# Kernel optimization log

Hardware: AMD Instinct MI355X
Metric: run time of the kernel (lower is better)

The kernel has to match this reference:

```python
import jax, jax.numpy as jnp
import numpy as np

ROIALIGN = (7, 7)   # args.roialign_size
SCALE = 0.125       # args.spatial_scale
SR = 2              # roi_align sampling ratio (fixed; torchvision uses adaptive when -1)


def _conv2d(x, w, b, pad):
    y = jax.lax.conv_general_dilated(x, w, (1, 1), pad,
                                     dimension_numbers=('NCHW', 'OIHW', 'NCHW'))
    return y + b[None, :, None, None]


def _bilinear(f, ys, xs):
    # f: [C,H,W]; ys: [Ny]; xs: [Nx] -> [C,Ny,Nx]
    C, H, W = f.shape
    y = jnp.clip(ys, 0.0, H - 1.0)
    x = jnp.clip(xs, 0.0, W - 1.0)
    y0 = jnp.floor(y).astype(jnp.int32)
    x0 = jnp.floor(x).astype(jnp.int32)
    y1 = jnp.minimum(y0 + 1, H - 1)
    x1 = jnp.minimum(x0 + 1, W - 1)
    wy = (y - y0)[None, :, None]
    wx = (x - x0)[None, None, :]
    f00 = f[:, y0[:, None], x0[None, :]]
    f01 = f[:, y0[:, None], x1[None, :]]
    f10 = f[:, y1[:, None], x0[None, :]]
    f11 = f[:, y1[:, None], x1[None, :]]
    return f00 * (1 - wy) * (1 - wx) + f01 * (1 - wy) * wx + f10 * wy * (1 - wx) + f11 * wy * wx


def _roi_align(feat, rois):
    # feat: [N,C,H,W]; rois: [K,5] = (batch_idx, x1, y1, x2, y2) in image coords
    rh, rw = ROIALIGN
    C = feat.shape[1]

    def one(box, bidx):
        f = feat[bidx]
        x1, y1, x2, y2 = box * SCALE
        bh = (y2 - y1) / rh
        bw = (x2 - x1) / rw
        ys = y1 + (jnp.arange(rh * SR, dtype=feat.dtype) + 0.5) / SR * bh
        xs = x1 + (jnp.arange(rw * SR, dtype=feat.dtype) + 0.5) / SR * bw
        s = _bilinear(f, ys, xs)                       # [C, rh*SR, rw*SR]
        return s.reshape(C, rh, SR, rw, SR).mean(axis=(2, 4))

    return jax.vmap(one)(rois[:, 1:5], rois[:, 0].astype(jnp.int32))


def setup_inputs() -> dict:
    key = jax.random.key(0)
    ks = jax.random.split(key, 16)
    N, M, H, W = 4, 48, 96, 96
    cor_planes = 4 * (2 * 4 + 1) ** 2  # 324
    corr = jax.random.normal(ks[0], (N, cor_planes, H, W), jnp.float32)

    def make_det(k):
        k1, k2, k3, k4, k5, k6 = jax.random.split(k, 6)
        cx = jax.random.uniform(k1, (N, M), minval=80.0, maxval=688.0)
        cy = jax.random.uniform(k2, (N, M), minval=80.0, maxval=688.0)
        w = jax.random.uniform(k3, (N, M), minval=24.0, maxval=120.0)
        h = jax.random.uniform(k4, (N, M), minval=24.0, maxval=120.0)
        valid = jnp.where(jax.random.uniform(k5, (N, M)) < 0.9, 1.0, -1.0)
        ids = jax.random.randint(k6, (N, M), 0, 100).astype(jnp.float32)
        pad = jnp.zeros((N, M, 4), jnp.float32)
        cols = [valid, ids, cx, cy, w, h]
        return jnp.concatenate([c[..., None] for c in cols] + [pad], axis=-1)

    detection1 = make_det(ks[1])
    detection2 = make_det(ks[2])

    def p(k, shape):
        return (jax.random.normal(k, shape, jnp.float32) * 0.02)

    return {
        'corr': corr,
        'detection1_': detection1,
        'detection1': detection1,
        'detection2': detection2,
        'convc1_w': p(ks[3], (256, cor_planes, 1, 1)), 'convc1_b': jnp.zeros(256, jnp.float32),
        'convc2_w': p(ks[4], (256, 256, 3, 3)), 'convc2_b': jnp.zeros(256, jnp.float32),
        'conv_w': p(ks[5], (128, 256, 3, 3)), 'conv_b': jnp.zeros(128, jnp.float32),
        'head_conv_w': p(ks[6], (256, 132, 7, 7)), 'head_conv_b': jnp.zeros(256, jnp.float32),
        'fc6_w': p(ks[7], (256, 256)), 'fc6_b': jnp.zeros(256, jnp.float32),
        'fc7_w': p(ks[8], (256, 256)), 'fc7_b': jnp.zeros(256, jnp.float32),
        'cls_w': p(ks[9], (1, 256)), 'cls_b': jnp.zeros(1, jnp.float32),
    }


def reference(corr, detection1_, detection1, detection2,
              convc1_w, convc1_b, convc2_w, convc2_b, conv_w, conv_b,
              head_conv_w, head_conv_b, fc6_w, fc6_b, fc7_w, fc7_b, cls_w, cls_b):
    N, M = detection1.shape[0], detection1.shape[1]
    rh, rw = ROIALIGN
    # CompressConv
    c = jax.nn.relu(_conv2d(corr, convc1_w, convc1_b, 'VALID'))
    c = jax.nn.relu(_conv2d(c, convc2_w, convc2_b, [(1, 1), (1, 1)]))
    rel = jax.nn.relu(_conv2d(c, conv_w, conv_b, [(1, 1), (1, 1)]))   # [N,128,H,W]

    def to_xyxy(d):
        xy1 = d[..., 2:4] - d[..., 4:6] / 2
        xy2 = xy1 + d[..., 4:6]
        return jnp.concatenate([d[..., :2], xy1, xy2, d[..., 6:]], axis=-1)

    d1 = to_xyxy(detection1)
    d2 = to_xyxy(detection2)
    bidx = jnp.broadcast_to(jnp.arange(N, dtype=d1.dtype)[:, None], (N, M))
    rois = jnp.concatenate([bidx[..., None], d1[..., 2:6]], axis=-1).reshape(N * M, 5)
    rf = _roi_align(rel, rois)                                        # [N*M,128,7,7]

    d_ = jnp.concatenate([
        jnp.broadcast_to(d1[..., :8][:, :, None, :], (N, M, M, 8)),
        jnp.broadcast_to(d2[..., :8][:, None, :, :], (N, M, M, 8)),
    ], axis=-1).reshape(N * M * M, 16)

    # position encoding: 4 relative-geometry channels tiled over the ROI grid
    eps = 1e-6
    cx1 = (d_[:, 2] + d_[:, 4]) * 0.5; cy1 = (d_[:, 3] + d_[:, 5]) * 0.5
    w1 = jnp.maximum(d_[:, 4] - d_[:, 2], eps); h1 = jnp.maximum(d_[:, 5] - d_[:, 3], eps)
    cx2 = (d_[:, 10] + d_[:, 12]) * 0.5; cy2 = (d_[:, 11] + d_[:, 13]) * 0.5
    w2 = jnp.maximum(d_[:, 12] - d_[:, 10], eps); h2 = jnp.maximum(d_[:, 13] - d_[:, 11], eps)
    pos4 = jnp.stack([(cx2 - cx1) / w1, (cy2 - cy1) / h1,
                      jnp.log(w2 / w1), jnp.log(h2 / h1)], axis=-1)   # [NMM,4]
    pos = jnp.broadcast_to(pos4[:, :, None, None], (N * M * M, 4, rh, rw))

    rf_exp = jnp.broadcast_to(rf[:, None], (N * M, M, 128, rh, rw)).reshape(N * M * M, 128, rh, rw)
    data = jnp.concatenate([rf_exp, pos], axis=1)                     # [NMM,132,7,7]

    labels = (d_[:, 1] == d_[:, 9]).astype(jnp.float32)
    valid = (d_[:, 0] != -1) & (d_[:, 8] != -1)

    # ConvMLPHead (scores for invalid pairs are simply masked out by `valid`)
    x = _conv2d(data, head_conv_w, head_conv_b, 'VALID').reshape(N * M * M, -1)
    x = jax.nn.relu(x @ fc6_w.T + fc6_b)
    x = jax.nn.relu(x @ fc7_w.T + fc7_b)
    scores = x @ cls_w.T + cls_b                                      # [NMM,1]
    return scores, labels, valid
```

## Files before the change

kernel.cpp:

```cpp
#include <hip/hip_runtime.h>
#include <hip/hip_bf16.h>

#define NB    4
#define HH    96
#define WW    96
#define PIX   9216
#define C0    324
#define MM    48
#define NROI  192
#define NPAIR 9216
#define KHEAD 6468
#define KRF   6272
#define SPLITS 28
#define CPS    7

#define CWSTG 18432

typedef unsigned short u16;
typedef __attribute__((ext_vector_type(8))) short bf16x8;
typedef __attribute__((ext_vector_type(4))) float f32x4;
typedef __attribute__((ext_vector_type(16))) float f32x16;
typedef __attribute__((ext_vector_type(4))) unsigned short u16x4;
typedef __attribute__((ext_vector_type(8))) unsigned short u16x8;
typedef __attribute__((ext_vector_type(4))) int i32x4;

__device__ __forceinline__ u16 f2bf(float f) {
    __hip_bfloat16 h = __float2bfloat16(f);
    union { __hip_bfloat16 h; u16 u; } c; c.h = h; return c.u;
}
__device__ __forceinline__ float b2f(u16 u) {
    union { unsigned int i; float f; } c; c.i = ((unsigned int)u) << 16; return c.f;
}

__global__ __launch_bounds__(256) void prep_v2(
    const float* __restrict__ c1w, const float* __restrict__ c2w,
    const float* __restrict__ c3w, const float* __restrict__ hw,
    const float* __restrict__ f6w, const float* __restrict__ f7w,
    u16* __restrict__ wt1f, u16* __restrict__ wt2f, u16* __restrict__ wt3f,
    u16* __restrict__ wtHt, u16* __restrict__ w6c, u16* __restrict__ w7c,
    float* __restrict__ wsum4, u16* __restrict__ a1, u16* __restrict__ a2)
{
    __shared__ u16 L[18432];
    const int blk = blockIdx.x, tid = threadIdx.x;

    if (blk < 8) {
        const int ot = blk;
        const float* src = c1w + (size_t)ot * 32 * C0;
        for (int it = 0; it < 11; ++it) {
            int i = tid + it * 256;
            if (i < 2592) {
                float4 v = *(const float4*)(src + i * 4);
                int n = i / 81, k4 = (i % 81) * 4;
                L[n * 324 + k4 + 0] = f2bf(v.x);
                L[n * 324 + k4 + 1] = f2bf(v.y);
                L[n * 324 + k4 + 2] = f2bf(v.z);
                L[n * 324 + k4 + 3] = f2bf(v.w);
            }
        }
        __syncthreads();
        for (int it = 0; it < 6; ++it) {
            int v = tid + it * 256;
            if (v >= 1408) break;
            int ks = v >> 6, lane = v & 63;
            int n = lane & 31, half = lane >> 5;
            u16x8 pk;
            #pragma unroll
            for (int j = 0; j < 8; ++j) {
                int k = ks * 16 + half * 8 + j;
                pk[j] = (k < C0) ? L[n * 324 + k] : (u16)0;
            }
            *(u16x8*)&wt1f[((ks * 8 + ot) * 64 + lane) * 8] = pk;
        }
    } else if (blk < 56) {
        const bool is2 = blk < 40;
        const int b8 = is2 ? (blk - 8) : (blk - 40);
        const int oc8 = b8 * 8;
        const int ocb = oc8 >> 7;
        const int ot = (oc8 >> 5) & 3;
        const int nb = oc8 & 31;
        const float* src = (is2 ? c2w : c3w) + (size_t)oc8 * 2304;
        u16* dst = is2 ? wt2f : wt3f;
        for (int it = 0; it < 18; ++it) {
            int i = tid + it * 256;
            float4 v = *(const float4*)(src + i * 4);
            int n = i / 576, t4 = (i % 576) * 4;
            L[n * 2304 + t4 + 0] = f2bf(v.x);
            L[n * 2304 + t4 + 1] = f2bf(v.y);
            L[n * 2304 + t4 + 2] = f2bf(v.z);
            L[n * 2304 + t4 + 3] = f2bf(v.w);
        }
        __syncthreads();
        for (int it = 0; it < 9; ++it) {
            int v = tid + it * 256;
            int o8 = v & 7; int rest = v >> 3;
            int half = rest & 1; rest >>= 1;
            int tap = rest % 9; int icb = rest / 9;
            int lane = half * 32 + nb + o8;
            u16x8 pk;
            #pragma unroll
            for (int j = 0; j < 8; ++j) {
                int ic = icb * 16 + half * 8 + j;
                pk[j] = L[o8 * 2304 + ic * 9 + tap];
            }
            size_t dest = ((((size_t)(ocb * 16 + icb) * 9 + tap) * 4 + ot) * 64 + lane) * 8;
            *(u16x8*)&dst[dest] = pk;
        }
    } else if (blk < 312) {
        const int oc = blk - 56;
        const float* src = hw + (size_t)oc * KHEAD;
        for (int it = 0; it < 7; ++it) {
            int i = tid + it * 256;
            if (i < 1617) {
                float4 v = *(const float4*)(src + i * 4);
                L[i * 4 + 0] = f2bf(v.x);
                L[i * 4 + 1] = f2bf(v.y);
                L[i * 4 + 2] = f2bf(v.z);
                L[i * 4 + 3] = f2bf(v.w);
            }
        }
        if (tid < 4) {
            const float* p = src + (128 + tid) * 49;
            float s = 0.f;
            #pragma unroll
            for (int t = 0; t < 49; ++t) s += p[t];
            wsum4[oc * 4 + tid] = s;
        }
        __syncthreads();
        for (int it = 0; it < 4; ++it) {
            int v = tid + it * 256;
            if (v >= 784) break;
            u16x8 pk;
            #pragma unroll
            for (int j = 0; j < 8; ++j) {
                int r = v * 8 + j;
                int s = r >> 7, c = r & 127;
                pk[j] = L[c * 49 + s];
            }
            *(u16x8*)&wtHt[(size_t)oc * KRF + v * 8] = pk;
        }
    } else if (blk < 344) {
        const bool is6 = blk < 328;
        const int b = is6 ? (blk - 312) : (blk - 328);
        const float* src = (is6 ? f6w : f7w) + (size_t)(b * 256 + tid) * 16;
        u16* dst = (is6 ? w6c : w7c) + (size_t)(b * 256 + tid) * 16;
        u16x8 pk0, pk1;
        #pragma unroll
        for (int h = 0; h < 2; ++h) {
            float4 v0 = *(const float4*)(src + h * 8);
            float4 v1 = *(const float4*)(src + h * 8 + 4);
            u16x8 pk;
            pk[0] = f2bf(v0.x); pk[1] = f2bf(v0.y); pk[2] = f2bf(v0.z); pk[3] = f2bf(v0.w);
            pk[4] = f2bf(v1.x); pk[5] = f2bf(v1.y); pk[6] = f2bf(v1.z); pk[7] = f2bf(v1.w);
            if (h == 0) pk0 = pk; else pk1 = pk;
        }
        *(u16x8*)(dst + 0) = pk0;
        *(u16x8*)(dst + 8) = pk1;
    } else {
        int idx = (blk - 344) * 256 + tid;
        int c8 = idx & 31;
        int t = idx >> 5;
        int h = t % 388, img = t / 388;
        u16* base = (img & 4) ? a2 : a1;
        int b = img & 3;
        int y, x;
        if (h < 98)       { y = 0;  x = h; }
        else if (h < 196) { y = 97; x = h - 98; }
        else { int r = (h - 196) >> 1; x = ((h - 196) & 1) * 97; y = 1 + r; }
        long long off = (((long long)(b * 98 + y)) * 98 + x) * 256 + c8 * 8;
        i32x4 z = {0, 0, 0, 0};
        *(i32x4*)(base + off) = z;
    }
}

__global__ __launch_bounds__(256) void conv1_v2(
    const float* __restrict__ corr, const u16* __restrict__ wf,
    const float* __restrict__ bias, u16* __restrict__ outp)
{
    __shared__ __align__(16) u16 Ws1[8192];
    __shared__ __align__(16) u16 Bs[64 * 40];
    const int tid = threadIdx.x;
    const int b = blockIdx.y;
    const int p0 = blockIdx.x * 64;
    const int lane = tid & 63, wid = tid >> 6;
    const int n = lane & 31, half = lane >> 5;
    const int wocw = wid & 1, wpx = wid >> 1;
    const int kr = tid >> 3, pxg = tid & 7;

    f32x16 acc[4];
    #pragma unroll
    for (int i = 0; i < 4; ++i)
        #pragma unroll
        for (int e = 0; e < 16; ++e) acc[i][e] = 0.f;

    float4 s0 = {0,0,0,0}, s1 = {0,0,0,0};
    if (kr < C0) {
        const float* src = &corr[((long long)(b * C0 + kr)) * PIX + p0 + pxg * 8];
        s0 = *(const float4*)src; s1 = *(const float4*)(src + 4);
    }
    bf16x8 wr[4];
    #pragma unroll
    for (int i = 0; i < 4; ++i) wr[i] = *(const bf16x8*)(wf + (i * 256 + tid) * 8);

    for (int kc = 0; kc < 11; ++kc) {
        __syncthreads();
        Bs[(pxg * 8 + 0) * 40 + kr] = f2bf(s0.x);
        Bs[(pxg * 8 + 1) * 40 + kr] = f2bf(s0.y);
        Bs[(pxg * 8 + 2) * 40 + kr] = f2bf(s0.z);
        Bs[(pxg * 8 + 3) * 40 + kr] = f2bf(s0.w);
        Bs[(pxg * 8 + 4) * 40 + kr] = f2bf(s1.x);
        Bs[(pxg * 8 + 5) * 40 + kr] = f2bf(s1.y);
        Bs[(pxg * 8 + 6) * 40 + kr] = f2bf(s1.z);
        Bs[(pxg * 8 + 7) * 40 + kr] = f2bf(s1.w);
        #pragma unroll
        for (int i = 0; i < 4; ++i) *(bf16x8*)&Ws1[(i * 256 + tid) * 8] = wr[i];
        __syncthreads();
        if (kc < 10) {
            int k = (kc + 1) * 32 + kr;
            if (k < C0) {
                const float* src = &corr[((long long)(b * C0 + k)) * PIX + p0 + pxg * 8];
                s0 = *(const float4*)src; s1 = *(const float4*)(src + 4);
            } else { s0 = (float4){0,0,0,0}; s1 = (float4){0,0,0,0}; }
            const u16* wn = wf + (kc + 1) * 8192;
            #pragma unroll
            for (int i = 0; i < 4; ++i) wr[i] = *(const bf16x8*)(wn + (i * 256 + tid) * 8);
        }
        #pragma unroll
        for (int ks = 0; ks < 2; ++ks) {
            bf16x8 bb = *(const bf16x8*)&Bs[(wpx * 32 + n) * 40 + ks * 16 + half * 8];
            #pragma unroll
            for (int ot = 0; ot < 4; ++ot) {
                bf16x8 a = *(const bf16x8*)&Ws1[((ks * 8 + wocw * 4 + ot) * 64 + lane) * 8];
                acc[ot] = __builtin_amdgcn_mfma_f32_32x32x16_bf16(a, bb, acc[ot], 0, 0, 0);
            }
        }
    }
    const int px = p0 + wpx * 32 + n;
    const int y = px / 96, x = px % 96;
    const long long obase = (((long long)(b * 98 + y + 1)) * 98 + x + 1) * 256;
    #pragma unroll
    for (int ot = 0; ot < 4; ++ot) {
        int ocb = wocw * 128 + ot * 32;
        f32x16 d = acc[ot];
        #pragma unroll
        for (int r2 = 0; r2 < 4; ++r2) {
            int oc4 = ocb + r2 * 8 + half * 4;
            f32x4 bv = *(const f32x4*)(bias + oc4);
            u16x4 pk;
            #pragma unroll
            for (int g = 0; g < 4; ++g) pk[g] = f2bf(fmaxf(d[r2 * 4 + g] + bv[g], 0.f));
            *(u16x4*)(outp + obase + oc4) = pk;
        }
    }
}

template<int COUT, bool PADOUT>
__global__ __launch_bounds__(256, 2) void conv3x3_v3(
    const u16* __restrict__ inp, const u16* __restrict__ wf,
    const float* __restrict__ bias, u16* __restrict__ outp)
{
    __shared__ __align__(16) u16 Ws[CWSTG];
    __shared__ __align__(16) u16 Hs[204 * 24];
    const int tid = threadIdx.x;
    const int b = blockIdx.z;
    const int x0 = (blockIdx.x % 3) * 32, y0 = (blockIdx.x / 3) * 4;
    const int lane = tid & 63, wid = tid >> 6;
    const int n = lane & 31, half = lane >> 5;
    const int woc = wid & 1, wpx = wid >> 1;

    const u16* wsrc = wf + (size_t)blockIdx.y * 16 * CWSTG;
    const bool hstager = tid < 204;
    const int hrow = tid / 34, hcol = tid % 34;
    const u16* hsrc = inp + (((size_t)(b * 98 + y0 + hrow)) * 98 + x0 + hcol) * 256;

    f32x16 acc[2][2];
    #pragma unroll
    for (int i = 0; i < 2; ++i)
        #pragma unroll
        for (int r = 0; r < 2; ++r)
            #pragma unroll
            for (int e = 0; e < 16; ++e) acc[i][r][e] = 0.f;

    bf16x8 wreg[9];
    bf16x8 h0, h1;
    #pragma unroll
    for (int it = 0; it < 9; ++it)
        wreg[it] = *(const bf16x8*)(wsrc + (it * 256 + tid) * 8);
    if (hstager) { h0 = *(const bf16x8*)hsrc; h1 = *(const bf16x8*)(hsrc + 8); }

    for (int icb = 0; icb < 16; ++icb) {
        __syncthreads();
        #pragma unroll
        for (int it = 0; it < 9; ++it)
            *(bf16x8*)&Ws[(it * 256 + tid) * 8] = wreg[it];
        if (hstager) {
            *(bf16x8*)&Hs[tid * 24]     = h0;
            *(bf16x8*)&Hs[tid * 24 + 8] = h1;
        }
        __syncthreads();
        if (icb < 15) {
            const u16* wn = wsrc + (size_t)(icb + 1) * CWSTG;
            #pragma unroll
            for (int it = 0; it < 9; ++it)
                wreg[it] = *(const bf16x8*)(wn + (it * 256 + tid) * 8);
            if (hstager) {
                const u16* hn = hsrc + (icb + 1) * 16;
                h0 = *(const bf16x8*)hn; h1 = *(const bf16x8*)(hn + 8);
            }
        }
        bf16x8 afr[9][2];
        #pragma unroll
        for (int tap = 0; tap < 9; ++tap)
            #pragma unroll
            for (int j = 0; j < 2; ++j)
                afr[tap][j] = *(const bf16x8*)&Ws[((tap * 4 + woc * 2 + j) * 64 + lane) * 8];
        bf16x8 bfr[4][3];
        #pragma unroll
        for (int rr = 0; rr < 4; ++rr)
            #pragma unroll
            for (int dx = 0; dx < 3; ++dx)
                bfr[rr][dx] = *(const bf16x8*)&Hs[((wpx * 2 + rr) * 34 + dx + n) * 24 + half * 8];
        #pragma unroll
        for (int tap = 0; tap < 9; ++tap) {
            const int dy = tap / 3, dx = tap % 3;
            #pragma unroll
            for (int r = 0; r < 2; ++r) {
                acc[0][r] = __builtin_amdgcn_mfma_f32_32x32x16_bf16(afr[tap][0], bfr[r + dy][dx], acc[0][r], 0, 0, 0);
                acc[1][r] = __builtin_amdgcn_mfma_f32_32x32x16_bf16(afr[tap][1], bfr[r + dy][dx], acc[1][r], 0, 0, 0);
            }
        }
    }
    #pragma unroll
    for (int ot = 0; ot < 2; ++ot) {
        int ocb = blockIdx.y * 128 + woc * 64 + ot * 32;
        #pragma unroll
        for (int r = 0; r < 2; ++r) {
            int y = y0 + wpx * 2 + r;
            int x = x0 + n;
            f32x16 d = acc[ot][r];
            long long obase;
            if (PADOUT) obase = (((long long)(b * 98 + y + 1)) * 98 + x + 1) * COUT;
            else        obase = (((long long)(b * 96 + y)) * 96 + x) * COUT;
            #pragma unroll
            for (int r2 = 0; r2 < 4; ++r2) {
                int oc4 = ocb + r2 * 8 + half * 4;
                f32x4 bv = *(const f32x4*)(bias + oc4);
                u16x4 pk;
                #pragma unroll
                for (int g = 0; g < 4; ++g) pk[g] = f2bf(fmaxf(d[r2 * 4 + g] + bv[g], 0.f));
                *(u16x4*)(outp + obase + oc4) = pk;
            }
        }
    }
}

__global__ __launch_bounds__(256) void roi_align_cl(
    const u16* __restrict__ rel, const float* __restrict__ det1,
    u16* __restrict__ rf)
{
    const int roi = blockIdx.x, tid = threadIdx.x;
    const int c = tid & 127, sb = tid >> 7;
    const int b = roi / MM, m = roi % MM;
    const float* d = det1 + (long long)(b * MM + m) * 10;
    float cx = d[2], cy = d[3], w = d[4], h = d[5];
    float x1f = cx - w * 0.5f, y1f = cy - h * 0.5f;
    float x1 = x1f * 0.125f, y1 = y1f * 0.125f;
    float x2 = (x1f + w) * 0.125f, y2 = (y1f + h) * 0.125f;
    float bh = (y2 - y1) * (1.f / 7.f), bw = (x2 - x1) * (1.f / 7.f);
    const u16* fb = rel + (long long)b * PIX * 128 + c;
    for (int s = sb; s < 49; s += 2) {
        int i = s / 7, j = s % 7;
        float sum = 0.f;
        #pragma unroll
        for (int di = 0; di < 2; ++di) {
            float y = y1 + ((float)(2 * i + di) + 0.5f) * 0.5f * bh;
            y = fminf(fmaxf(y, 0.f), 95.f);
            int yy0 = (int)floorf(y);
            int yy1 = min(yy0 + 1, 95);
            float wy = y - (float)yy0;
            #pragma unroll
            for (int dj = 0; dj < 2; ++dj) {
                float x = x1 + ((float)(2 * j + dj) + 0.5f) * 0.5f * bw;
                x = fminf(fmaxf(x, 0.f), 95.f);
                int xx0 = (int)floorf(x);
                int xx1 = min(xx0 + 1, 95);
                float wx = x - (float)xx0;
                float f00 = b2f(fb[((long long)yy0 * 96 + xx0) * 128]);
                float f01 = b2f(fb[((long long)yy0 * 96 + xx1) * 128]);
                float f10 = b2f(fb[((long long)yy1 * 96 + xx0) * 128]);
                float f11 = b2f(fb[((long long)yy1 * 96 + xx1) * 128]);
                sum += f00 * (1.f - wy) * (1.f - wx) + f01 * (1.f - wy) * wx
                     + f10 * wy * (1.f - wx) + f11 * wy * wx;
            }
        }
        rf[(long long)roi * KRF + s * 128 + c] = f2bf(sum * 0.25f);
    }
}

__global__ __launch_bounds__(256) void head_gemm_mfma(
    const u16* __restrict__ rf, const u16* __restrict__ wtHt,
    float* __restrict__ Gpart)
{
    __shared__ __align__(16) u16 As[64 * 40];
    __shared__ __align__(16) u16 Bs[128 * 40];
    const int tid = threadIdx.x;
    const int rb = blockIdx.x >> 1, ob = blockIdx.x & 1;
    const int split = blockIdx.y;
    const int lane = tid & 63, wid = tid >> 6;
    const int q = lane >> 4, m16 = lane & 15;
    const int wr = wid & 1, wo = wid >> 1;

    const int arl = tid >> 2, aqd = tid & 3;
    const u16* abase = rf + (long long)(rb * 64 + arl) * KRF + aqd * 8;
    const int bol0 = tid >> 2, bqd = tid & 3;
    const u16* bbase0 = wtHt + (long long)(ob * 128 + bol0) * KRF + bqd * 8;
    const u16* bbase1 = bbase0 + 64LL * KRF;

    f32x4 acc[2][4];
    #pragma unroll
    for (int i = 0; i < 2; ++i)
        #pragma unroll
        for (int j = 0; j < 4; ++j) acc[i][j] = (f32x4){0.f, 0.f, 0.f, 0.f};

    int k0 = split * CPS * 32;
    bf16x8 ra = *(const bf16x8*)(abase + k0);
    bf16x8 rb0 = *(const bf16x8*)(bbase0 + k0);
    bf16x8 rb1 = *(const bf16x8*)(bbase1 + k0);
    for (int cch = 0; cch < CPS; ++cch) {
        __syncthreads();
        *(bf16x8*)&As[arl * 40 + aqd * 8] = ra;
        *(bf16x8*)&Bs[bol0 * 40 + bqd * 8] = rb0;
        *(bf16x8*)&Bs[(64 + bol0) * 40 + bqd * 8] = rb1;
        __syncthreads();
        if (cch < CPS - 1) {
            int kn = k0 + (cch + 1) * 32;
            ra  = *(const bf16x8*)(abase + kn);
            rb0 = *(const bf16x8*)(bbase0 + kn);
            rb1 = *(const bf16x8*)(bbase1 + kn);
        }
        bf16x8 a[2], bb[4];
        #pragma unroll
        for (int rt = 0; rt < 2; ++rt)
            a[rt] = *(const bf16x8*)&As[(wr * 32 + rt * 16 + m16) * 40 + q * 8];
        #pragma unroll
        for (int ot = 0; ot < 4; ++ot)
            bb[ot] = *(const bf16x8*)&Bs[(wo * 64 + ot * 16 + m16) * 40 + q * 8];
        #pragma unroll
        for (int rt = 0; rt < 2; ++rt)
            #pragma unroll
            for (int ot = 0; ot < 4; ++ot)
                acc[rt][ot] = __builtin_amdgcn_mfma_f32_16x16x32_bf16(a[rt], bb[ot], acc[rt][ot], 0, 0, 0);
    }
    #pragma unroll
    for (int rt = 0; rt < 2; ++rt)
        #pragma unroll
        for (int ot = 0; ot < 4; ++ot) {
            int oc = ob * 128 + wo * 64 + ot * 16 + m16;
            #pragma unroll
            for (int rg = 0; rg < 4; ++rg) {
                int roi = rb * 64 + wr * 32 + rt * 16 + q * 4 + rg;
                Gpart[((long long)split * NROI + roi) * 256 + oc] = acc[rt][ot][rg];
            }
        }
}

#define PHS 272
__global__ __launch_bounds__(256) void pair_head(
    const float* __restrict__ Gpart, const float* __restrict__ d1,
    const float* __restrict__ d2, const float* __restrict__ wsum4,
    const float* __restrict__ hb,
    const u16* __restrict__ w6, const float* __restrict__ b6,
    const u16* __restrict__ w7, const float* __restrict__ b7,
    const float* __restrict__ cw, const float* __restrict__ cb,
    float* __restrict__ scores, float* __restrict__ labels,
    float* __restrict__ valid)
{
    __shared__ __align__(16) u16 bufA[64 * PHS];
    __shared__ __align__(16) u16 bufB[64 * PHS];
    __shared__ float Gs[2][256];
    __shared__ float ps[64][4];
    __shared__ float clw[256];

    const int tid = threadIdx.x;
    const int p0 = blockIdx.x * 64;
    const int r0 = p0 / MM;
    const int lane = tid & 63, w = tid >> 6;
    const int q = lane >> 4, m16 = lane & 15;

    clw[tid] = cw[tid];
    #pragma unroll
    for (int l = 0; l < 2; ++l) {
        int idx = tid + l * 256;
        int rr = idx >> 8, col = idx & 255;
        int roi = min(r0 + rr, NROI - 1);
        float s = 0.f;
        #pragma unroll
        for (int sp = 0; sp < SPLITS; ++sp)
            s += Gpart[((long long)sp * NROI + roi) * 256 + col];
        Gs[rr][col] = s;
    }
    if (tid < 64) {
        int pair = p0 + tid;
        int b = pair / (MM * MM); int rem = pair % (MM * MM);
        int m1 = rem / MM, m2 = rem % MM;
        const float* rA = d1 + (long long)(b * MM + m1) * 10;
        const float* rB = d2 + (long long)(b * MM + m2) * 10;
        float v1 = rA[0], id1 = rA[1], cxa = rA[2], cya = rA[3], wa = rA[4], ha = rA[5];
        float v2 = rB[0], id2 = rB[1], cxb = rB[2], cyb = rB[3], wb = rB[4], hbv = rB[5];
        const float eps = 1e-6f;
        float ax1 = cxa - wa * 0.5f, ay1 = cya - ha * 0.5f;
        float ax2 = ax1 + wa,        ay2 = ay1 + ha;
        float bx1 = cxb - wb * 0.5f, by1 = cyb - hbv * 0.5f;
        float bx2 = bx1 + wb,        by2 = by1 + hbv;
        float ccx1 = (ax1 + ax2) * 0.5f, ccy1 = (ay1 + ay2) * 0.5f;
        float ww1 = fmaxf(ax2 - ax1, eps), hh1 = fmaxf(ay2 - ay1, eps);
        float ccx2 = (bx1 + bx2) * 0.5f, ccy2 = (by1 + by2) * 0.5f;
        float ww2 = fmaxf(bx2 - bx1, eps), hh2 = fmaxf(by2 - by1, eps);
        ps[tid][0] = (ccx2 - ccx1) / ww1;
        ps[tid][1] = (ccy2 - ccy1) / hh1;
        ps[tid][2] = logf(ww2 / ww1);
        ps[tid][3] = logf(hh2 / hh1);
        labels[pair] = (id1 == id2) ? 1.f : 0.f;
        valid[pair]  = (v1 != -1.f && v2 != -1.f) ? 1.f : 0.f;
    }
    __syncthreads();

    #pragma unroll
    for (int it = 0; it < 16; ++it) {
        int idx = tid + it * 256;
        int px = idx >> 6, o4 = (idx & 63) * 4;
        int rl = (p0 + px) / MM - r0;
        f32x4 g = *(const f32x4*)&Gs[rl][o4];
        f32x4 hv = *(const f32x4*)&hb[o4];
        f32x4 p4 = *(const f32x4*)&ps[px][0];
        u16x4 pk;
        #pragma unroll
        for (int j = 0; j < 4; ++j) {
            f32x4 w4 = *(const f32x4*)&wsum4[(o4 + j) * 4];
            float v = g[j] + hv[j] + p4[0] * w4[0] + p4[1] * w4[1] + p4[2] * w4[2] + p4[3] * w4[3];
            pk[j] = f2bf(v);
        }
        *(u16x4*)&bufA[px * PHS + o4] = pk;
    }
    __syncthreads();

    #pragma unroll
    for (int layer = 0; layer < 2; ++layer) {
        const u16* wgt = layer ? w7 : w6;
        const float* bs = layer ? b7 : b6;
        const u16* src = layer ? bufB : bufA;
        u16* dst = layer ? bufA : bufB;
        f32x4 acc[4][4];
        #pragma unroll
        for (int i = 0; i < 4; ++i)
            #pragma unroll
            for (int j = 0; j < 4; ++j) acc[i][j] = (f32x4){0.f, 0.f, 0.f, 0.f};
        #pragma unroll
        for (int kc = 0; kc < 8; ++kc) {
            bf16x8 a[4], bb[4];
            #pragma unroll
            for (int i = 0; i < 4; ++i)
                a[i] = *(const bf16x8*)&wgt[(w * 64 + i * 16 + m16) * 256 + kc * 32 + q * 8];
            #pragma unroll
            for (int pt = 0; pt < 4; ++pt)
                bb[pt] = *(const bf16x8*)&src[(pt * 16 + m16) * PHS + kc * 32 + q * 8];
            #pragma unroll
            for (int i = 0; i < 4; ++i)
                #pragma unroll
                for (int pt = 0; pt < 4; ++pt)
                    acc[i][pt] = __builtin_amdgcn_mfma_f32_16x16x32_bf16(a[i], bb[pt], acc[i][pt], 0, 0, 0);
        }
        #pragma unroll
        for (int i = 0; i < 4; ++i) {
            int oc4 = w * 64 + i * 16 + q * 4;
            f32x4 bv = *(const f32x4*)(bs + oc4);
            #pragma unroll
            for (int pt = 0; pt < 4; ++pt) {
                int px = pt * 16 + m16;
                f32x4 dd = acc[i][pt];
                u16x4 pk;
                #pragma unroll
                for (int rg = 0; rg < 4; ++rg)
                    pk[rg] = f2bf(fmaxf(dd[rg] + bv[rg], 0.f));
                *(u16x4*)&dst[px * PHS + oc4] = pk;
            }
        }
        __syncthreads();
    }

    {
        int px = tid >> 2, qq = tid & 3;
        float acc = 0.f;
        #pragma unroll
        for (int k8 = 0; k8 < 8; ++k8) {
            bf16x8 hv = *(const bf16x8*)&bufA[px * PHS + qq * 64 + k8 * 8];
            #pragma unroll
            for (int e = 0; e < 8; ++e)
                acc += b2f((u16)hv[e]) * clw[qq * 64 + k8 * 8 + e];
        }
        acc += __shfl_xor(acc, 1, 64);
        acc += __shfl_xor(acc, 2, 64);
        if (qq == 0) scores[p0 + px] = acc + cb[0];
    }
}

extern "C" void kernel_launch(void* const* d_in, const int* in_sizes, int n_in,
                              void* d_out, int out_size, void* d_ws, size_t ws_size,
                              hipStream_t stream) {
    const float* corr   = (const float*)d_in[0];
    const float* det1   = (const float*)d_in[2];
    const float* det2   = (const float*)d_in[3];
    const float* c1w    = (const float*)d_in[4];
    const float* c1b    = (const float*)d_in[5];
    const float* c2w    = (const float*)d_in[6];
    const float* c2b    = (const float*)d_in[7];
    const float* c3w    = (const float*)d_in[8];
    const float* c3b    = (const float*)d_in[9];
    const float* hw     = (const float*)d_in[10];
    const float* hbias  = (const float*)d_in[11];
    const float* f6w    = (const float*)d_in[12];
    const float* f6b    = (const float*)d_in[13];
    const float* f7w    = (const float*)d_in[14];
    const float* f7b    = (const float*)d_in[15];
    const float* clsw   = (const float*)d_in[16];
    const float* clsb   = (const float*)d_in[17];
    float* out = (float*)d_out;

    char* base = (char*)d_ws;
    auto alloc = [&](size_t bytes) { char* p = base; base += (bytes + 255) & ~(size_t)255; return p; };

    const size_t ACTP_BYTES = (size_t)NB * 98 * 98 * 256 * 2;
    u16*   act1p = (u16*)  alloc(ACTP_BYTES);
    u16*   act2p = (u16*)  alloc(ACTP_BYTES);
    u16*   rel   = (u16*)  alloc((size_t)NB * PIX * 128 * 2);
    u16*   wt1f  = (u16*)  alloc((size_t)90112 * 2);
    u16*   wt2f  = (u16*)  alloc((size_t)2 * 16 * CWSTG * 2);
    u16*   wt3f  = (u16*)  alloc((size_t)16 * CWSTG * 2);
    u16*   wtHt  = (u16*)  alloc((size_t)256 * KRF * 2);
    u16*   w6c   = (u16*)  alloc(256 * 256 * 2);
    u16*   w7c   = (u16*)  alloc(256 * 256 * 2);
    float* wsum4 = (float*)alloc(256 * 4 * 4);
    u16*   rf    = (u16*)  alloc((size_t)NROI * KRF * 2);
    float* Gpart = (float*)alloc((size_t)SPLITS * NROI * 256 * 4);

    float* scores_out = out;
    float* labels_out = out + NPAIR;
    float* valid_out  = out + 2 * NPAIR;

    prep_v2<<<732, 256, 0, stream>>>(c1w, c2w, c3w, hw, f6w, f7w,
                                     wt1f, wt2f, wt3f, wtHt, w6c, w7c, wsum4,
                                     act1p, act2p);
    conv1_v2<<<dim3(144, NB), 256, 0, stream>>>(corr, wt1f, c1b, act1p);
    conv3x3_v3<256, true><<<dim3(72, 2, NB), 256, 0, stream>>>(act1p, wt2f, c2b, act2p);
    conv3x3_v3<128, false><<<dim3(72, 1, NB), 256, 0, stream>>>(act2p, wt3f, c3b, rel);
    roi_align_cl<<<NROI, 256, 0, stream>>>(rel, det1, rf);
    head_gemm_mfma<<<dim3(6, SPLITS), 256, 0, stream>>>(rf, wtHt, Gpart);
    pair_head<<<144, 256, 0, stream>>>(Gpart, det1, det2, wsum4, hbias,
                                       w6c, f6b, w7c, f7b, clsw, clsb,
                                       scores_out, labels_out, valid_out);
}
```

Before: 282.3 us.

## Double conv3x3 spatial tile height and remap conv1 staging threads for coalescing

The 3x3 conv kernels now compute 8 output rows per block instead of 4. This halves the grid and doubles the MFMA work per staged weight tile, so weight global loads and LDS traffic are amortised over more pixels. B fragments are loaded per dx column and reused across dy taps to keep register pressure manageable. conv1 swaps the thread mapping so consecutive threads read different channels (kr = tid&31) rather than consecutive pixel groups. The risks are fewer blocks (288 and 144), which may underfill the GPU, and higher accumulator register use that could hurt occupancy at 2 blocks per CU.

```diff
diff --git a/kernel.cpp b/kernel.cpp
--- a/kernel.cpp
+++ b/kernel.cpp
@@ -172,7 +172,7 @@
     }
 }
 
-__global__ __launch_bounds__(256) void conv1_v2(
+__global__ __launch_bounds__(256) void conv1_v3(
     const float* __restrict__ corr, const u16* __restrict__ wf,
     const float* __restrict__ bias, u16* __restrict__ outp)
 {
@@ -184,7 +184,7 @@
     const int lane = tid & 63, wid = tid >> 6;
     const int n = lane & 31, half = lane >> 5;
     const int wocw = wid & 1, wpx = wid >> 1;
-    const int kr = tid >> 3, pxg = tid & 7;
+    const int kr = tid & 31, pg = tid >> 5;
 
     f32x16 acc[4];
     #pragma unroll
@@ -193,8 +193,8 @@
         for (int e = 0; e < 16; ++e) acc[i][e] = 0.f;
 
     float4 s0 = {0,0,0,0}, s1 = {0,0,0,0};
-    if (kr < C0) {
-        const float* src = &corr[((long long)(b * C0 + kr)) * PIX + p0 + pxg * 8];
+    {
+        const float* src = &corr[((long long)(b * C0 + kr)) * PIX + p0 + pg * 8];
         s0 = *(const float4*)src; s1 = *(const float4*)(src + 4);
     }
     bf16x8 wr[4];
@@ -203,21 +203,21 @@
 
     for (int kc = 0; kc < 11; ++kc) {
         __syncthreads();
-        Bs[(pxg * 8 + 0) * 40 + kr] = f2bf(s0.x);
-        Bs[(pxg * 8 + 1) * 40 + kr] = f2bf(s0.y);
-        Bs[(pxg * 8 + 2) * 40 + kr] = f2bf(s0.z);
-        Bs[(pxg * 8 + 3) * 40 + kr] = f2bf(s0.w);
-        Bs[(pxg * 8 + 4) * 40 + kr] = f2bf(s1.x);
-        Bs[(pxg * 8 + 5) * 40 + kr] = f2bf(s1.y);
-        Bs[(pxg * 8 + 6) * 40 + kr] = f2bf(s1.z);
-        Bs[(pxg * 8 + 7) * 40 + kr] = f2bf(s1.w);
+        Bs[(pg * 8 + 0) * 40 + kr] = f2bf(s0.x);
+        Bs[(pg * 8 + 1) * 40 + kr] = f2bf(s0.y);
+        Bs[(pg * 8 + 2) * 40 + kr] = f2bf(s0.z);
+        Bs[(pg * 8 + 3) * 40 + kr] = f2bf(s0.w);
+        Bs[(pg * 8 + 4) * 40 + kr] = f2bf(s1.x);
+        Bs[(pg * 8 + 5) * 40 + kr] = f2bf(s1.y);
+        Bs[(pg * 8 + 6) * 40 + kr] = f2bf(s1.z);
+        Bs[(pg * 8 + 7) * 40 + kr] = f2bf(s1.w);
         #pragma unroll
         for (int i = 0; i < 4; ++i) *(bf16x8*)&Ws1[(i * 256 + tid) * 8] = wr[i];
         __syncthreads();
         if (kc < 10) {
             int k = (kc + 1) * 32 + kr;
             if (k < C0) {
-                const float* src = &corr[((long long)(b * C0 + k)) * PIX + p0 + pxg * 8];
+                const float* src = &corr[((long long)(b * C0 + k)) * PIX + p0 + pg * 8];
                 s0 = *(const float4*)src; s1 = *(const float4*)(src + 4);
             } else { s0 = (float4){0,0,0,0}; s1 = (float4){0,0,0,0}; }
             const u16* wn = wf + (kc + 1) * 8192;
@@ -254,47 +254,55 @@
 }
 
 template<int COUT, bool PADOUT>
-__global__ __launch_bounds__(256, 2) void conv3x3_v3(
+__global__ __launch_bounds__(256, 2) void conv3x3_v4(
     const u16* __restrict__ inp, const u16* __restrict__ wf,
     const float* __restrict__ bias, u16* __restrict__ outp)
 {
     __shared__ __align__(16) u16 Ws[CWSTG];
-    __shared__ __align__(16) u16 Hs[204 * 24];
+    __shared__ __align__(16) u16 Hs[340 * 24];
     const int tid = threadIdx.x;
     const int b = blockIdx.z;
-    const int x0 = (blockIdx.x % 3) * 32, y0 = (blockIdx.x / 3) * 4;
+    const int x0 = (blockIdx.x % 3) * 32, y0 = (blockIdx.x / 3) * 8;
     const int lane = tid & 63, wid = tid >> 6;
     const int n = lane & 31, half = lane >> 5;
     const int woc = wid & 1, wpx = wid >> 1;
 
     const u16* wsrc = wf + (size_t)blockIdx.y * 16 * CWSTG;
-    const bool hstager = tid < 204;
-    const int hrow = tid / 34, hcol = tid % 34;
-    const u16* hsrc = inp + (((size_t)(b * 98 + y0 + hrow)) * 98 + x0 + hcol) * 256;
-
-    f32x16 acc[2][2];
+    const bool hst = tid < 170;
+    const int h0 = tid, h1 = tid + 170;
+    const int r0 = h0 / 34, c0 = h0 % 34;
+    const int r1 = h1 / 34, c1 = h1 % 34;
+    const u16* hsrc0 = inp + (((size_t)(b * 98 + y0 + r0)) * 98 + x0 + c0) * 256;
+    const u16* hsrc1 = inp + (((size_t)(b * 98 + y0 + r1)) * 98 + x0 + c1) * 256;
+
+    f32x16 acc[2][4];
     #pragma unroll
     for (int i = 0; i < 2; ++i)
         #pragma unroll
-        for (int r = 0; r < 2; ++r)
+        for (int r = 0; r < 4; ++r)
             #pragma unroll
             for (int e = 0; e < 16; ++e) acc[i][r][e] = 0.f;
 
     bf16x8 wreg[9];
-    bf16x8 h0, h1;
+    bf16x8 ha0, ha1, hb0, hb1;
     #pragma unroll
     for (int it = 0; it < 9; ++it)
         wreg[it] = *(const bf16x8*)(wsrc + (it * 256 + tid) * 8);
-    if (hstager) { h0 = *(const bf16x8*)hsrc; h1 = *(const bf16x8*)(hsrc + 8); }
+    if (hst) {
+        ha0 = *(const bf16x8*)hsrc0; ha1 = *(const bf16x8*)(hsrc0 + 8);
+        hb0 = *(const bf16x8*)hsrc1; hb1 = *(const bf16x8*)(hsrc1 + 8);
+    }
 
     for (int icb = 0; icb < 16; ++icb) {
         __syncthreads();
         #pragma unroll
         for (int it = 0; it < 9; ++it)
             *(bf16x8*)&Ws[(it * 256 + tid) * 8] = wreg[it];
-        if (hstager) {
-            *(bf16x8*)&Hs[tid * 24]     = h0;
-            *(bf16x8*)&Hs[tid * 24 + 8] = h1;
+        if (hst) {
+            *(bf16x8*)&Hs[h0 * 24]     = ha0;
+            *(bf16x8*)&Hs[h0 * 24 + 8] = ha1;
+            *(bf16x8*)&Hs[h1 * 24]     = hb0;
+            *(bf16x8*)&Hs[h1 * 24 + 8] = hb1;
         }
         __syncthreads();
         if (icb < 15) {
@@ -302,30 +310,29 @@
             #pragma unroll
             for (int it = 0; it < 9; ++it)
                 wreg[it] = *(const bf16x8*)(wn + (it * 256 + tid) * 8);
-            if (hstager) {
-                const u16* hn = hsrc + (icb + 1) * 16;
-                h0 = *(const bf16x8*)hn; h1 = *(const bf16x8*)(hn + 8);
-            }
-        }
-        bf16x8 afr[9][2];
-        #pragma unroll
-        for (int tap = 0; tap < 9; ++tap)
-            #pragma unroll
-            for (int j = 0; j < 2; ++j)
-                afr[tap][j] = *(const bf16x8*)&Ws[((tap * 4 + woc * 2 + j) * 64 + lane) * 8];
-        bf16x8 bfr[4][3];
-        #pragma unroll
-        for (int rr = 0; rr < 4; ++rr)
-            #pragma unroll
-            for (int dx = 0; dx < 3; ++dx)
-                bfr[rr][dx] = *(const bf16x8*)&Hs[((wpx * 2 + rr) * 34 + dx + n) * 24 + half * 8];
-        #pragma unroll
-        for (int tap = 0; tap < 9; ++tap) {
-            const int dy = tap / 3, dx = tap % 3;
-            #pragma unroll
-            for (int r = 0; r < 2; ++r) {
-                acc[0][r] = __builtin_amdgcn_mfma_f32_32x32x16_bf16(afr[tap][0], bfr[r + dy][dx], acc[0][r], 0, 0, 0);
-                acc[1][r] = __builtin_amdgcn_mfma_f32_32x32x16_bf16(afr[tap][1], bfr[r + dy][dx], acc[1][r], 0, 0, 0);
+            if (hst) {
+                const u16* p0n = hsrc0 + (icb + 1) * 16;
+                const u16* p1n = hsrc1 + (icb + 1) * 16;
+                ha0 = *(const bf16x8*)p0n; ha1 = *(const bf16x8*)(p0n + 8);
+                hb0 = *(const bf16x8*)p1n; hb1 = *(const bf16x8*)(p1n + 8);
+            }
+        }
+        #pragma unroll
+        for (int dx = 0; dx < 3; ++dx) {
+            bf16x8 B[6];
+            #pragma unroll
+            for (int j = 0; j < 6; ++j)
+                B[j] = *(const bf16x8*)&Hs[((wpx * 4 + j) * 34 + n + dx) * 24 + half * 8];
+            #pragma unroll
+            for (int dyi = 0; dyi < 3; ++dyi) {
+                const int tap = dyi * 3 + dx;
+                bf16x8 A0 = *(const bf16x8*)&Ws[((tap * 4 + woc * 2 + 0) * 64 + lane) * 8];
+                bf16x8 A1 = *(const bf16x8*)&Ws[((tap * 4 + woc * 2 + 1) * 64 + lane) * 8];
+                #pragma unroll
+                for (int r = 0; r < 4; ++r) {
+                    acc[0][r] = __builtin_amdgcn_mfma_f32_32x32x16_bf16(A0, B[r + dyi], acc[0][r], 0, 0, 0);
+                    acc[1][r] = __builtin_amdgcn_mfma_f32_32x32x16_bf16(A1, B[r + dyi], acc[1][r], 0, 0, 0);
+                }
             }
         }
     }
@@ -333,8 +340,8 @@
     for (int ot = 0; ot < 2; ++ot) {
         int ocb = blockIdx.y * 128 + woc * 64 + ot * 32;
         #pragma unroll
-        for (int r = 0; r < 2; ++r) {
-            int y = y0 + wpx * 2 + r;
+        for (int r = 0; r < 4; ++r) {
+            int y = y0 + wpx * 4 + r;
             int x = x0 + n;
             f32x16 d = acc[ot][r];
             long long obase;
@@ -649,9 +656,9 @@
     prep_v2<<<732, 256, 0, stream>>>(c1w, c2w, c3w, hw, f6w, f7w,
                                      wt1f, wt2f, wt3f, wtHt, w6c, w7c, wsum4,
                                      act1p, act2p);
-    conv1_v2<<<dim3(144, NB), 256, 0, stream>>>(corr, wt1f, c1b, act1p);
-    conv3x3_v3<256, true><<<dim3(72, 2, NB), 256, 0, stream>>>(act1p, wt2f, c2b, act2p);
-    conv3x3_v3<128, false><<<dim3(72, 1, NB), 256, 0, stream>>>(act2p, wt3f, c3b, rel);
+    conv1_v3<<<dim3(144, NB), 256, 0, stream>>>(corr, wt1f, c1b, act1p);
+    conv3x3_v4<256, true><<<dim3(36, 2, NB), 256, 0, stream>>>(act1p, wt2f, c2b, act2p);
+    conv3x3_v4<128, false><<<dim3(36, 1, NB), 256, 0, stream>>>(act2p, wt3f, c3b, rel);
     roi_align_cl<<<NROI, 256, 0, stream>>>(rel, det1, rf);
     head_gemm_mfma<<<dim3(6, SPLITS), 256, 0, stream>>>(rf, wtHt, Gpart);
     pair_head<<<144, 256, 0, stream>>>(Gpart, det1, det2, wsum4, hbias,
```

Measured after the change: 289.0 us. +2.4%, slower.
